# Performance work log

Measured on AMD Instinct MI355X. Metric: run time of the kernel, lower is better.

The kernel has to match this reference:

```python
import jax, jax.numpy as jnp
import numpy as np

N_NODES = 100000
N_EDGES = 1600000
IN_FEATS = 64
HIDDEN = 64
NUM_CLASSES = 40


def setup_inputs() -> dict:
    key = jax.random.key(0)
    ks = jax.random.split(key, 8)
    x = jax.random.normal(ks[0], (N_NODES, IN_FEATS), dtype=jnp.float32)
    edge_index = jax.random.randint(ks[1], (2, N_EDGES), 0, N_NODES, dtype=jnp.int64)
    s = 1.0 / np.sqrt(IN_FEATS)
    W1_l = jax.random.uniform(ks[2], (HIDDEN, IN_FEATS), jnp.float32, -s, s)
    b1 = jnp.zeros((HIDDEN,), jnp.float32)
    W1_r = jax.random.uniform(ks[3], (HIDDEN, IN_FEATS), jnp.float32, -s, s)
    s2 = 1.0 / np.sqrt(HIDDEN)
    W2_l = jax.random.uniform(ks[4], (NUM_CLASSES, HIDDEN), jnp.float32, -s2, s2)
    b2 = jnp.zeros((NUM_CLASSES,), jnp.float32)
    W2_r = jax.random.uniform(ks[5], (NUM_CLASSES, HIDDEN), jnp.float32, -s2, s2)
    return {"x": x, "edge_index": edge_index, "W1_l": W1_l, "b1": b1,
            "W1_r": W1_r, "W2_l": W2_l, "b2": b2, "W2_r": W2_r}


def _sage_conv(x, src, dst, Wl, b, Wr, num_nodes):
    # mean aggregation of source-node features onto target nodes
    msg = x[src]                                           # [E, d] gather
    agg = jax.ops.segment_sum(msg, dst, num_segments=num_nodes)   # [N, d]
    deg = jax.ops.segment_sum(jnp.ones((src.shape[0],), x.dtype), dst,
                              num_segments=num_nodes)      # [N]
    agg = agg / jnp.maximum(deg, 1.0)[:, None]
    # out = lin_l(agg) + lin_r(x)  (PyG SAGEConv: root weight, bias on lin_l)
    return agg @ Wl.T + b + x @ Wr.T


def reference(x, edge_index, W1_l, b1, W1_r, W2_l, b2, W2_r):
    n = x.shape[0]
    src, dst = edge_index[0], edge_index[1]
    h = _sage_conv(x, src, dst, W1_l, b1, W1_r, n)
    h = jax.nn.relu(h)
    # dropout p=0.5 only active in training; reference runs eval mode (identity)
    return _sage_conv(h, src, dst, W2_l, b2, W2_r, n)
```

## Files before the change

kernel.cpp:

```cpp
#include <hip/hip_runtime.h>

#define N_NODES 100000
#define N_EDGES 1600000
#define NCLS 40
#define BIN_SH 8
#define BIN_N 256
#define NBIN ((N_NODES + BIN_N - 1) / BIN_N)
#define BINCAP 4800
#define BKBLK 256
#define BKTHR 1024
#define CHUNK (N_EDGES / BKBLK)
#define SENTINEL N_NODES
#define NN1 (N_NODES + 1)

typedef __attribute__((ext_vector_type(8))) short s8v;
typedef __attribute__((ext_vector_type(4))) float f4v;
typedef __attribute__((ext_vector_type(2))) float f2v;

__device__ __forceinline__ unsigned short f2bf(float f) {
    union { float f; unsigned int u; } v; v.f = f;
    unsigned int u = v.u + 0x7FFFu + ((v.u >> 16) & 1u);
    return (unsigned short)(u >> 16);
}
__device__ __forceinline__ float blo(unsigned int u) {
    union { unsigned int u; float f; } v; v.u = u << 16; return v.f;
}
__device__ __forceinline__ float bhi(unsigned int u) {
    union { unsigned int u; float f; } v; v.u = u & 0xFFFF0000u; return v.f;
}

#if __has_builtin(__builtin_amdgcn_cvt_pk_fp8_f32) && __has_builtin(__builtin_amdgcn_cvt_f32_fp8)
#define FP8_HW 1
#else
#define FP8_HW 0
#endif
#if __has_builtin(__builtin_amdgcn_cvt_pk_f32_fp8)
#define FP8_PK 1
#else
#define FP8_PK 0
#endif

__device__ __forceinline__ unsigned char enc_e4m3_sw(float f) {
    union { float f; unsigned int u; } v; v.f = f;
    unsigned int s = (v.u >> 24) & 0x80u;
    float af = fabsf(f);
    if (af >= 448.0f) return (unsigned char)(s | 0x7E);
    if (af < 0.015625f) {
        int q = (int)rintf(af * 512.0f);
        return (unsigned char)(s | (q & 7));
    }
    unsigned int n = v.u & 0x7FFFFFFFu;
    n = n + 0x7FFFFu + ((n >> 20) & 1u);
    int e = (int)(n >> 23) - 120;
    unsigned int m = (n >> 20) & 7u;
    if (e <= 0) { int q = (int)rintf(af * 512.0f); return (unsigned char)(s | (q & 7)); }
    if (e > 15) return (unsigned char)(s | 0x7E);
    return (unsigned char)(s | (e << 3) | m);
}
__device__ __forceinline__ float dec_e4m3_sw(unsigned int byte) {
    unsigned int sgn = byte >> 7, e = (byte >> 3) & 15u, m = byte & 7u;
    float mag;
    if (e) { union { unsigned int u; float f; } v; v.u = ((e + 120u) << 23) | (m << 20); mag = v.f; }
    else mag = (float)m * 0.001953125f;
    return sgn ? -mag : mag;
}

__device__ __forceinline__ unsigned int pack4_fp8(float a, float b, float c, float d) {
#if FP8_HW
    unsigned int w = __builtin_amdgcn_cvt_pk_fp8_f32(a, b, 0u, false);
    w = __builtin_amdgcn_cvt_pk_fp8_f32(c, d, w, true);
    return w;
#else
    return (unsigned int)enc_e4m3_sw(a) | ((unsigned int)enc_e4m3_sw(b) << 8) |
           ((unsigned int)enc_e4m3_sw(c) << 16) | ((unsigned int)enc_e4m3_sw(d) << 24);
#endif
}

__device__ __forceinline__ void acc_fp8pk(unsigned int w, f2v* a) {
#if FP8_PK
    a[0] += __builtin_amdgcn_cvt_pk_f32_fp8((int)w, false);
    a[1] += __builtin_amdgcn_cvt_pk_f32_fp8((int)w, true);
#else
    f2v lo, hi;
    lo.x = dec_e4m3_sw(w & 255u);         lo.y = dec_e4m3_sw((w >> 8) & 255u);
    hi.x = dec_e4m3_sw((w >> 16) & 255u); hi.y = dec_e4m3_sw(w >> 24);
    a[0] += lo; a[1] += hi;
#endif
}
__device__ __forceinline__ void acc_fp8x16(uint4 u, f2v* a) {
    acc_fp8pk(u.x, a + 0); acc_fp8pk(u.y, a + 2);
    acc_fp8pk(u.z, a + 4); acc_fp8pk(u.w, a + 6);
}

__global__ __launch_bounds__(BKTHR) void k_bucket(
        const int* __restrict__ srcv, const int* __restrict__ dstv,
        int* __restrict__ bcur, int* __restrict__ bedges) {
    __shared__ int cnt4[4][NBIN];
    __shared__ int base[NBIN], lcur[NBIN];
    for (int i = threadIdx.x; i < 4 * NBIN; i += BKTHR) cnt4[i / NBIN][i % NBIN] = 0;
    __syncthreads();
    const int grp = threadIdx.x >> 8;
    const int beg = blockIdx.x * CHUNK;
    const int end = beg + CHUNK;
    for (int e = beg + threadIdx.x; e < end; e += BKTHR) {
        int d = dstv[e]; d = min(max(d, 0), N_NODES - 1);
        atomicAdd(&cnt4[grp][d >> BIN_SH], 1);
    }
    __syncthreads();
    for (int i = threadIdx.x; i < NBIN; i += BKTHR) {
        int c = cnt4[0][i] + cnt4[1][i] + cnt4[2][i] + cnt4[3][i];
        base[i] = atomicAdd(&bcur[i], c);
        lcur[i] = 0;
    }
    __syncthreads();
    for (int e = beg + threadIdx.x; e < end; e += BKTHR) {
        int d = dstv[e]; d = min(max(d, 0), N_NODES - 1);
        int s = srcv[e]; s = min(max(s, 0), N_NODES - 1);
        int b = d >> BIN_SH;
        int slot = atomicAdd(&lcur[b], 1) + base[b];
        if (slot < BINCAP) bedges[b * BINCAP + slot] = ((d & (BIN_N - 1)) << 17) | s;
    }
}

__global__ __launch_bounds__(256) void k_csrfill(
        const int* __restrict__ bcur, const int* __restrict__ bedges,
        int* __restrict__ gcnt, uint2* __restrict__ offdeg,
        int* __restrict__ srcs) {
    __shared__ int dcnt[BIN_N];
    __shared__ int s[BIN_N];
    __shared__ int base_s;
    const int b = blockIdx.x;
    dcnt[threadIdx.x] = 0;
    __syncthreads();
    const int cnt = min(bcur[b], BINCAP);
    for (int e = threadIdx.x; e < cnt; e += 256)
        atomicAdd(&dcnt[bedges[b * BINCAP + e] >> 17], 1);
    __syncthreads();
    int v = dcnt[threadIdx.x];
    int pv = (v + 3) & ~3;
    s[threadIdx.x] = pv;
    __syncthreads();
    int acc = pv;
    for (int off = 1; off < 256; off <<= 1) {
        int t = (threadIdx.x >= off) ? s[threadIdx.x - off] : 0;
        __syncthreads();
        acc += t;
        s[threadIdx.x] = acc;
        __syncthreads();
    }
    if (threadIdx.x == 255) base_s = atomicAdd(gcnt, acc);
    __syncthreads();
    const int gbeg = (acc - pv) + base_s;
    const int node = (b << BIN_SH) + threadIdx.x;
    if (node < N_NODES) offdeg[node] = make_uint2((unsigned)gbeg, (unsigned)v);
    s[threadIdx.x] = gbeg;
    dcnt[threadIdx.x] = 0;
    __syncthreads();
    for (int e = threadIdx.x; e < cnt; e += 256) {
        int val = bedges[b * BINCAP + e];
        int dl = val >> 17;
        int sv = val & 0x1FFFF;
        int slot = atomicAdd(&dcnt[dl], 1);
        srcs[s[dl] + slot] = sv;
    }
    for (int p = v; p < pv; ++p) srcs[gbeg + p] = SENTINEL;
}

__global__ void k_xb(const float* __restrict__ x, unsigned int* __restrict__ xbs,
                     unsigned int* __restrict__ h2f8, unsigned int* __restrict__ xf8) {
    int i = blockIdx.x * blockDim.x + threadIdx.x;
    int stride = gridDim.x * blockDim.x;
    const int total = N_NODES * 8;
    for (int tt = i; tt < total; tt += stride) {
        int node = tt >> 3, sub = tt & 7;
        int slice = sub >> 1, half = sub & 1;
        float4 v0 = ((const float4*)x)[tt * 2];
        float4 v1 = ((const float4*)x)[tt * 2 + 1];
        uint4 o;
        o.x = (unsigned)f2bf(v0.x) | ((unsigned)f2bf(v0.y) << 16);
        o.y = (unsigned)f2bf(v0.z) | ((unsigned)f2bf(v0.w) << 16);
        o.z = (unsigned)f2bf(v1.x) | ((unsigned)f2bf(v1.y) << 16);
        o.w = (unsigned)f2bf(v1.z) | ((unsigned)f2bf(v1.w) << 16);
        ((uint4*)xbs)[((size_t)slice * NN1 + node) * 2 + half] = o;
        uint2 p;
        p.x = pack4_fp8(v0.x, v0.y, v0.z, v0.w);
        p.y = pack4_fp8(v1.x, v1.y, v1.z, v1.w);
        ((uint2*)xf8)[(size_t)node * 8 + sub] = p;
    }
    uint4 z; z.x = 0u; z.y = 0u; z.z = 0u; z.w = 0u;
    if (i < 8) {
        int slice = i >> 1, half = i & 1;
        ((uint4*)xbs)[((size_t)slice * NN1 + N_NODES) * 2 + half] = z;
    }
    if (i >= 16 && i < 28) h2f8[(size_t)N_NODES * 16 + (i - 16)] = 0u;
    if (i >= 32 && i < 48) xf8[(size_t)N_NODES * 16 + (i - 32)] = 0u;
}

__global__ __launch_bounds__(256) void k_agg(
        const uint2* __restrict__ offdeg, const int* __restrict__ srcs,
        const unsigned int* __restrict__ xf8, unsigned short* __restrict__ aggs) {
    const int lane = threadIdx.x & 63;
    const int w = threadIdx.x >> 6;
    const int g = lane >> 4;
    const int c = (lane >> 2) & 3;
    const int t = lane & 3;
    const int wid = blockIdx.x * 4 + w;
    for (int nb = wid * 4; nb < N_NODES; nb += 32768) {
        const int node = nb + g;
        uint2 od = offdeg[node];
        const int beg = (int)od.x;
        const int m = ((int)od.y + 3) >> 2;
        f2v a2[8];
        #pragma unroll
        for (int k = 0; k < 8; ++k) { a2[k].x = 0.0f; a2[k].y = 0.0f; }
        int j = c;
        if (j < m) {
            int4 sv = *(const int4*)&srcs[beg + 4 * j];
            while (true) {
                const int4 cur = sv;
                const int jn = j + 4;
                if (jn < m) sv = *(const int4*)&srcs[beg + 4 * jn];
                uint4 u0 = *(const uint4*)&xf8[(size_t)cur.x * 16 + t * 4];
                uint4 u1 = *(const uint4*)&xf8[(size_t)cur.y * 16 + t * 4];
                uint4 u2 = *(const uint4*)&xf8[(size_t)cur.z * 16 + t * 4];
                uint4 u3 = *(const uint4*)&xf8[(size_t)cur.w * 16 + t * 4];
                acc_fp8x16(u0, a2); acc_fp8x16(u1, a2);
                acc_fp8x16(u2, a2); acc_fp8x16(u3, a2);
                if (jn >= m) break;
                j = jn;
            }
        }
        float* af = (float*)a2;
        #pragma unroll
        for (int k = 0; k < 16; ++k) {
            af[k] += __shfl_xor(af[k], 4, 64);
            af[k] += __shfl_xor(af[k], 8, 64);
        }
        if (c == 0) {
            float rd = 1.0f / fmaxf((float)od.y, 1.0f);
            uint4 r0, r1;
            r0.x = (unsigned)f2bf(af[0] * rd)  | ((unsigned)f2bf(af[1] * rd) << 16);
            r0.y = (unsigned)f2bf(af[2] * rd)  | ((unsigned)f2bf(af[3] * rd) << 16);
            r0.z = (unsigned)f2bf(af[4] * rd)  | ((unsigned)f2bf(af[5] * rd) << 16);
            r0.w = (unsigned)f2bf(af[6] * rd)  | ((unsigned)f2bf(af[7] * rd) << 16);
            r1.x = (unsigned)f2bf(af[8] * rd)  | ((unsigned)f2bf(af[9] * rd) << 16);
            r1.y = (unsigned)f2bf(af[10] * rd) | ((unsigned)f2bf(af[11] * rd) << 16);
            r1.z = (unsigned)f2bf(af[12] * rd) | ((unsigned)f2bf(af[13] * rd) << 16);
            r1.w = (unsigned)f2bf(af[14] * rd) | ((unsigned)f2bf(af[15] * rd) << 16);
            unsigned short* dst = &aggs[((size_t)t * NN1 + node) * 16];
            *(uint4*)dst = r0;
            *(uint4*)(dst + 8) = r1;
        }
    }
}

__global__ __launch_bounds__(256) void k_dense(
        const unsigned short* __restrict__ aggs, const unsigned short* __restrict__ xbs,
        const float* __restrict__ W1l, const float* __restrict__ b1,
        const float* __restrict__ W1r,
        const float* __restrict__ W2l, const float* __restrict__ b2,
        const float* __restrict__ W2r,
        unsigned int* __restrict__ h2f8, float* __restrict__ op) {
    __shared__ __align__(16) unsigned short wl1[64][72], wr1[64][72];
    __shared__ __align__(16) unsigned short wl2[48][72], wr2[48][72];
    __shared__ __align__(16) unsigned short hsm[4][16][72];
    for (int idx = threadIdx.x; idx < 64 * 64; idx += 256) {
        int f = idx >> 6, k = idx & 63;
        wl1[f][k] = f2bf(W1l[idx]);
        wr1[f][k] = f2bf(W1r[idx]);
    }
    for (int idx = threadIdx.x; idx < 48 * 64; idx += 256) {
        int c = idx >> 6, k = idx & 63;
        wl2[c][k] = (c < NCLS) ? f2bf(W2l[c * 64 + k]) : (unsigned short)0;
        wr2[c][k] = (c < NCLS) ? f2bf(W2r[c * 64 + k]) : (unsigned short)0;
    }
    __syncthreads();
    const int w   = threadIdx.x >> 6;
    const int l15 = threadIdx.x & 15;
    const int g   = (threadIdx.x >> 4) & 3;
    const size_t sLo = (size_t)(g >> 1) * NN1;
    const size_t sHi = (size_t)(2 + (g >> 1)) * NN1;
    const int off = (g & 1) * 8;
    float b1v[4][4], b2v[3][4];
    #pragma unroll
    for (int ft = 0; ft < 4; ++ft)
        #pragma unroll
        for (int r = 0; r < 4; ++r)
            b1v[ft][r] = b1[16 * ft + 4 * g + r];
    #pragma unroll
    for (int ct = 0; ct < 3; ++ct)
        #pragma unroll
        for (int r = 0; r < 4; ++r) {
            int c = 16 * ct + 4 * g + r;
            b2v[ct][r] = (c < NCLS) ? b2[c] : 0.0f;
        }
    unsigned short* hs = &hsm[w][0][0];
    const int gw = blockIdx.x * 4 + w;
    const int nw = gridDim.x * 4;
    for (int tile = gw; tile < N_NODES / 16; tile += nw) {
        const size_t node = (size_t)tile * 16 + l15;
        s8v aB0 = *(const s8v*)&aggs[(sLo + node) * 16 + off];
        s8v aB1 = *(const s8v*)&aggs[(sHi + node) * 16 + off];
        s8v xB0 = *(const s8v*)&xbs[(sLo + node) * 16 + off];
        s8v xB1 = *(const s8v*)&xbs[(sHi + node) * 16 + off];
        #pragma unroll
        for (int ft = 0; ft < 4; ++ft) {
            f4v c;
            c[0] = b1v[ft][0]; c[1] = b1v[ft][1]; c[2] = b1v[ft][2]; c[3] = b1v[ft][3];
            const size_t rb = (size_t)(16 * ft + l15) * 144 + 16 * g;
            s8v A0 = *(const s8v*)((const char*)wl1 + rb);
            s8v A1 = *(const s8v*)((const char*)wl1 + rb + 64);
            s8v R0 = *(const s8v*)((const char*)wr1 + rb);
            s8v R1 = *(const s8v*)((const char*)wr1 + rb + 64);
            c = __builtin_amdgcn_mfma_f32_16x16x32_bf16(A0, aB0, c, 0, 0, 0);
            c = __builtin_amdgcn_mfma_f32_16x16x32_bf16(A1, aB1, c, 0, 0, 0);
            c = __builtin_amdgcn_mfma_f32_16x16x32_bf16(R0, xB0, c, 0, 0, 0);
            c = __builtin_amdgcn_mfma_f32_16x16x32_bf16(R1, xB1, c, 0, 0, 0);
            uint2 u;
            u.x = (unsigned)f2bf(fmaxf(c[0], 0.0f)) | ((unsigned)f2bf(fmaxf(c[1], 0.0f)) << 16);
            u.y = (unsigned)f2bf(fmaxf(c[2], 0.0f)) | ((unsigned)f2bf(fmaxf(c[3], 0.0f)) << 16);
            *(uint2*)((char*)hs + l15 * 144 + 32 * ft + 8 * g) = u;
        }
        s8v hB0 = *(const s8v*)((const char*)hs + l15 * 144 + 16 * g);
        s8v hB1 = *(const s8v*)((const char*)hs + l15 * 144 + 64 + 16 * g);
        #pragma unroll
        for (int ct = 0; ct < 3; ++ct) {
            f4v p; p[0] = 0.0f; p[1] = 0.0f; p[2] = 0.0f; p[3] = 0.0f;
            f4v qv;
            qv[0] = b2v[ct][0]; qv[1] = b2v[ct][1]; qv[2] = b2v[ct][2]; qv[3] = b2v[ct][3];
            const size_t rb = (size_t)(16 * ct + l15) * 144 + 16 * g;
            s8v L0 = *(const s8v*)((const char*)wl2 + rb);
            s8v L1 = *(const s8v*)((const char*)wl2 + rb + 64);
            s8v Q0 = *(const s8v*)((const char*)wr2 + rb);
            s8v Q1 = *(const s8v*)((const char*)wr2 + rb + 64);
            p  = __builtin_amdgcn_mfma_f32_16x16x32_bf16(L0, hB0, p, 0, 0, 0);
            p  = __builtin_amdgcn_mfma_f32_16x16x32_bf16(L1, hB1, p, 0, 0, 0);
            qv = __builtin_amdgcn_mfma_f32_16x16x32_bf16(Q0, hB0, qv, 0, 0, 0);
            qv = __builtin_amdgcn_mfma_f32_16x16x32_bf16(Q1, hB1, qv, 0, 0, 0);
            int c0 = 16 * ct + 4 * g;
            h2f8[node * 16 + (4 * ct + g)] = pack4_fp8(p[0], p[1], p[2], p[3]);
            if (c0 < NCLS) {
                float4 o; o.x = qv[0]; o.y = qv[1]; o.z = qv[2]; o.w = qv[3];
                *(float4*)&op[node * NCLS + c0] = o;
            }
        }
    }
}

__global__ __launch_bounds__(256) void k_out(
        const uint2* __restrict__ offdeg, const int* __restrict__ srcs,
        const unsigned int* __restrict__ h2f8, float* __restrict__ out) {
    const int lane = threadIdx.x & 63;
    const int w = threadIdx.x >> 6;
    const int g = lane >> 4;
    const int q = (lane >> 2) & 3;
    const int t = lane & 3;
    const int wid = blockIdx.x * 4 + w;
    for (int nb = wid * 4; nb < N_NODES; nb += 32768) {
        const int node = nb + g;
        uint2 od = offdeg[node];
        const int beg = (int)od.x;
        const int m = ((int)od.y + 3) >> 2;
        f2v a2[8];
        #pragma unroll
        for (int k = 0; k < 8; ++k) { a2[k].x = 0.0f; a2[k].y = 0.0f; }
        if (t < 3) {
            int j = q;
            if (j < m) {
                int4 sv = *(const int4*)&srcs[beg + 4 * j];
                while (true) {
                    const int4 cur = sv;
                    const int jn = j + 4;
                    if (jn < m) sv = *(const int4*)&srcs[beg + 4 * jn];
                    uint4 u0 = *(const uint4*)&h2f8[(size_t)cur.x * 16 + t * 4];
                    uint4 u1 = *(const uint4*)&h2f8[(size_t)cur.y * 16 + t * 4];
                    uint4 u2 = *(const uint4*)&h2f8[(size_t)cur.z * 16 + t * 4];
                    uint4 u3 = *(const uint4*)&h2f8[(size_t)cur.w * 16 + t * 4];
                    acc_fp8x16(u0, a2); acc_fp8x16(u1, a2);
                    acc_fp8x16(u2, a2); acc_fp8x16(u3, a2);
                    if (jn >= m) break;
                    j = jn;
                }
            }
        }
        float* a = (float*)a2;
        #pragma unroll
        for (int k = 0; k < 16; ++k) {
            a[k] += __shfl_xor(a[k], 4, 64);
            a[k] += __shfl_xor(a[k], 8, 64);
        }
        if (q == 0 && t < 3) {
            float rd = 1.0f / fmaxf((float)od.y, 1.0f);
            const int base = t * 16;
            const int nwords = (t == 2) ? 2 : 4;
            #pragma unroll
            for (int i = 0; i < 4; ++i) {
                if (i < nwords) {
                    float4 o = *(float4*)&out[(size_t)node * NCLS + base + 4 * i];
                    o.x = fmaf(a[4 * i + 0], rd, o.x);
                    o.y = fmaf(a[4 * i + 1], rd, o.y);
                    o.z = fmaf(a[4 * i + 2], rd, o.z);
                    o.w = fmaf(a[4 * i + 3], rd, o.w);
                    *(float4*)&out[(size_t)node * NCLS + base + 4 * i] = o;
                }
            }
        }
    }
}

extern "C" void kernel_launch(void* const* d_in, const int* in_sizes, int n_in,
                              void* d_out, int out_size, void* d_ws, size_t ws_size,
                              hipStream_t stream) {
    const float* x   = (const float*)d_in[0];
    const int*   ei  = (const int*)d_in[1];
    const float* W1l = (const float*)d_in[2];
    const float* b1  = (const float*)d_in[3];
    const float* W1r = (const float*)d_in[4];
    const float* W2l = (const float*)d_in[5];
    const float* b2  = (const float*)d_in[6];
    const float* W2r = (const float*)d_in[7];
    float* out = (float*)d_out;

    const int* srcv = ei;
    const int* dstv = ei + N_EDGES;

    int* bcur   = (int*)d_ws;
    int* gcnt   = bcur + 508;
    uint2* offdeg = (uint2*)(bcur + 512);
    int* bedges = (int*)(offdeg + N_NODES);
    int* srcs   = bedges + (size_t)NBIN * BINCAP;
    unsigned short* aggs = (unsigned short*)(srcs + (size_t)N_EDGES + 3 * N_NODES + 16);
    unsigned short* xbs  = aggs + (size_t)64 * NN1;
    unsigned int*   h2f8 = (unsigned int*)(xbs + (size_t)64 * NN1);
    unsigned int*   xf8  = h2f8 + (size_t)16 * NN1;

    hipMemsetAsync(bcur, 0, 512 * sizeof(int), stream);
    k_bucket<<<BKBLK, BKTHR, 0, stream>>>(srcv, dstv, bcur, bedges);
    k_xb<<<2048, 256, 0, stream>>>(x, (unsigned int*)xbs, h2f8, xf8);
    k_csrfill<<<NBIN, 256, 0, stream>>>(bcur, bedges, gcnt, offdeg, srcs);
    k_agg<<<2048, 256, 0, stream>>>(offdeg, srcs, xf8, aggs);
    k_dense<<<768, 256, 0, stream>>>(aggs, xbs, W1l, b1, W1r, W2l, b2, W2r, h2f8, out);
    k_out<<<2048, 256, 0, stream>>>(offdeg, srcs, h2f8, out);
}
```

Measured before the change: 124.2 us.

## Replace bucketed CSR build with global-atomic degree count, scan, and scatter

Removes the two-level LDS bucket sort (bucket + per-bin CSR fill) and instead counts per-node degrees with global atomics fused into the feature conversion kernel. A per-block scan then computes padded offsets, and a scatter kernel places edges using global atomic cursors. This eliminates the intermediate bucket buffer and one kernel pass. In exchange it relies on millions of returning global atomics to random addresses and makes neighbor order nondeterministic.

```diff
diff --git a/kernel.cpp b/kernel.cpp
--- a/kernel.cpp
+++ b/kernel.cpp
@@ -3,13 +3,7 @@
 #define N_NODES 100000
 #define N_EDGES 1600000
 #define NCLS 40
-#define BIN_SH 8
-#define BIN_N 256
-#define NBIN ((N_NODES + BIN_N - 1) / BIN_N)
-#define BINCAP 4800
-#define BKBLK 256
-#define BKTHR 1024
-#define CHUNK (N_EDGES / BKBLK)
+#define NBIN ((N_NODES + 255) / 256)
 #define SENTINEL N_NODES
 #define NN1 (N_NODES + 1)
 
@@ -92,84 +86,16 @@
     acc_fp8pk(u.z, a + 4); acc_fp8pk(u.w, a + 6);
 }
 
-__global__ __launch_bounds__(BKTHR) void k_bucket(
-        const int* __restrict__ srcv, const int* __restrict__ dstv,
-        int* __restrict__ bcur, int* __restrict__ bedges) {
-    __shared__ int cnt4[4][NBIN];
-    __shared__ int base[NBIN], lcur[NBIN];
-    for (int i = threadIdx.x; i < 4 * NBIN; i += BKTHR) cnt4[i / NBIN][i % NBIN] = 0;
-    __syncthreads();
-    const int grp = threadIdx.x >> 8;
-    const int beg = blockIdx.x * CHUNK;
-    const int end = beg + CHUNK;
-    for (int e = beg + threadIdx.x; e < end; e += BKTHR) {
-        int d = dstv[e]; d = min(max(d, 0), N_NODES - 1);
-        atomicAdd(&cnt4[grp][d >> BIN_SH], 1);
-    }
-    __syncthreads();
-    for (int i = threadIdx.x; i < NBIN; i += BKTHR) {
-        int c = cnt4[0][i] + cnt4[1][i] + cnt4[2][i] + cnt4[3][i];
-        base[i] = atomicAdd(&bcur[i], c);
-        lcur[i] = 0;
-    }
-    __syncthreads();
-    for (int e = beg + threadIdx.x; e < end; e += BKTHR) {
-        int d = dstv[e]; d = min(max(d, 0), N_NODES - 1);
-        int s = srcv[e]; s = min(max(s, 0), N_NODES - 1);
-        int b = d >> BIN_SH;
-        int slot = atomicAdd(&lcur[b], 1) + base[b];
-        if (slot < BINCAP) bedges[b * BINCAP + slot] = ((d & (BIN_N - 1)) << 17) | s;
-    }
-}
-
-__global__ __launch_bounds__(256) void k_csrfill(
-        const int* __restrict__ bcur, const int* __restrict__ bedges,
-        int* __restrict__ gcnt, uint2* __restrict__ offdeg,
-        int* __restrict__ srcs) {
-    __shared__ int dcnt[BIN_N];
-    __shared__ int s[BIN_N];
-    __shared__ int base_s;
-    const int b = blockIdx.x;
-    dcnt[threadIdx.x] = 0;
-    __syncthreads();
-    const int cnt = min(bcur[b], BINCAP);
-    for (int e = threadIdx.x; e < cnt; e += 256)
-        atomicAdd(&dcnt[bedges[b * BINCAP + e] >> 17], 1);
-    __syncthreads();
-    int v = dcnt[threadIdx.x];
-    int pv = (v + 3) & ~3;
-    s[threadIdx.x] = pv;
-    __syncthreads();
-    int acc = pv;
-    for (int off = 1; off < 256; off <<= 1) {
-        int t = (threadIdx.x >= off) ? s[threadIdx.x - off] : 0;
-        __syncthreads();
-        acc += t;
-        s[threadIdx.x] = acc;
-        __syncthreads();
-    }
-    if (threadIdx.x == 255) base_s = atomicAdd(gcnt, acc);
-    __syncthreads();
-    const int gbeg = (acc - pv) + base_s;
-    const int node = (b << BIN_SH) + threadIdx.x;
-    if (node < N_NODES) offdeg[node] = make_uint2((unsigned)gbeg, (unsigned)v);
-    s[threadIdx.x] = gbeg;
-    dcnt[threadIdx.x] = 0;
-    __syncthreads();
-    for (int e = threadIdx.x; e < cnt; e += 256) {
-        int val = bedges[b * BINCAP + e];
-        int dl = val >> 17;
-        int sv = val & 0x1FFFF;
-        int slot = atomicAdd(&dcnt[dl], 1);
-        srcs[s[dl] + slot] = sv;
-    }
-    for (int p = v; p < pv; ++p) srcs[gbeg + p] = SENTINEL;
-}
-
-__global__ void k_xb(const float* __restrict__ x, unsigned int* __restrict__ xbs,
-                     unsigned int* __restrict__ h2f8, unsigned int* __restrict__ xf8) {
+__global__ __launch_bounds__(256) void k_degxb(
+        const int* __restrict__ dstv, const float* __restrict__ x,
+        int* __restrict__ deg, unsigned int* __restrict__ xbs,
+        unsigned int* __restrict__ h2f8, unsigned int* __restrict__ xf8) {
     int i = blockIdx.x * blockDim.x + threadIdx.x;
     int stride = gridDim.x * blockDim.x;
+    for (int e = i; e < N_EDGES; e += stride) {
+        int d = dstv[e]; d = min(max(d, 0), N_NODES - 1);
+        atomicAdd(&deg[d], 1);
+    }
     const int total = N_NODES * 8;
     for (int tt = i; tt < total; tt += stride) {
         int node = tt >> 3, sub = tt & 7;
@@ -194,6 +120,48 @@
     }
     if (i >= 16 && i < 28) h2f8[(size_t)N_NODES * 16 + (i - 16)] = 0u;
     if (i >= 32 && i < 48) xf8[(size_t)N_NODES * 16 + (i - 32)] = 0u;
+}
+
+__global__ __launch_bounds__(256) void k_scan(
+        const int* __restrict__ deg, int* __restrict__ gcnt,
+        uint2* __restrict__ offdeg, int* __restrict__ cur,
+        int* __restrict__ srcs) {
+    __shared__ int s[256];
+    __shared__ int base_s;
+    const int node = (blockIdx.x << 8) + threadIdx.x;
+    int v = (node < N_NODES) ? deg[node] : 0;
+    int pv = (v + 3) & ~3;
+    s[threadIdx.x] = pv;
+    __syncthreads();
+    int acc = pv;
+    for (int off = 1; off < 256; off <<= 1) {
+        int t = (threadIdx.x >= off) ? s[threadIdx.x - off] : 0;
+        __syncthreads();
+        acc += t;
+        s[threadIdx.x] = acc;
+        __syncthreads();
+    }
+    if (threadIdx.x == 255) base_s = atomicAdd(gcnt, acc);
+    __syncthreads();
+    const int gbeg = (acc - pv) + base_s;
+    if (node < N_NODES) {
+        offdeg[node] = make_uint2((unsigned)gbeg, (unsigned)v);
+        cur[node] = gbeg;
+        for (int p = v; p < pv; ++p) srcs[gbeg + p] = SENTINEL;
+    }
+}
+
+__global__ __launch_bounds__(256) void k_scatter(
+        const int* __restrict__ srcv, const int* __restrict__ dstv,
+        int* __restrict__ cur, int* __restrict__ srcs) {
+    int i = blockIdx.x * blockDim.x + threadIdx.x;
+    int stride = gridDim.x * blockDim.x;
+    for (int e = i; e < N_EDGES; e += stride) {
+        int d = dstv[e]; d = min(max(d, 0), N_NODES - 1);
+        int s = srcv[e]; s = min(max(s, 0), N_NODES - 1);
+        int slot = atomicAdd(&cur[d], 1);
+        srcs[slot] = s;
+    }
 }
 
 __global__ __launch_bounds__(256) void k_agg(
@@ -424,20 +392,20 @@
     const int* srcv = ei;
     const int* dstv = ei + N_EDGES;
 
-    int* bcur   = (int*)d_ws;
-    int* gcnt   = bcur + 508;
-    uint2* offdeg = (uint2*)(bcur + 512);
-    int* bedges = (int*)(offdeg + N_NODES);
-    int* srcs   = bedges + (size_t)NBIN * BINCAP;
+    int* deg    = (int*)d_ws;
+    int* cur    = deg + N_NODES;
+    int* gcnt   = cur + N_NODES;
+    uint2* offdeg = (uint2*)(deg + 2 * N_NODES + 2);
+    int* srcs   = (int*)(offdeg + N_NODES);
     unsigned short* aggs = (unsigned short*)(srcs + (size_t)N_EDGES + 3 * N_NODES + 16);
     unsigned short* xbs  = aggs + (size_t)64 * NN1;
     unsigned int*   h2f8 = (unsigned int*)(xbs + (size_t)64 * NN1);
     unsigned int*   xf8  = h2f8 + (size_t)16 * NN1;
 
-    hipMemsetAsync(bcur, 0, 512 * sizeof(int), stream);
-    k_bucket<<<BKBLK, BKTHR, 0, stream>>>(srcv, dstv, bcur, bedges);
-    k_xb<<<2048, 256, 0, stream>>>(x, (unsigned int*)xbs, h2f8, xf8);
-    k_csrfill<<<NBIN, 256, 0, stream>>>(bcur, bedges, gcnt, offdeg, srcs);
+    hipMemsetAsync(deg, 0, (2 * N_NODES + 2) * sizeof(int), stream);
+    k_degxb<<<2048, 256, 0, stream>>>(dstv, x, deg, (unsigned int*)xbs, h2f8, xf8);
+    k_scan<<<NBIN, 256, 0, stream>>>(deg, gcnt, offdeg, cur, srcs);
+    k_scatter<<<2048, 256, 0, stream>>>(srcv, dstv, cur, srcs);
     k_agg<<<2048, 256, 0, stream>>>(offdeg, srcs, xf8, aggs);
     k_dense<<<768, 256, 0, stream>>>(aggs, xbs, W1l, b1, W1r, W2l, b2, W2r, h2f8, out);
     k_out<<<2048, 256, 0, stream>>>(offdeg, srcs, h2f8, out);
```

Result: slower. 293.1 us (+135.9%).
